# Kernel tuning notes

Measured on AMD Instinct MI355X. Metric: run time of the kernel, lower is better.

The kernel has to match this reference:

```python
import jax, jax.numpy as jnp
import numpy as np

D_MODEL = 1024
NUM_HEADS = 16
HEAD_DIM = D_MODEL // NUM_HEADS


def setup_inputs() -> dict:
    key = jax.random.key(0)
    k1, k2, k3, k4, k5 = jax.random.split(key, 5)
    B, S = 2, 2048
    X = jax.random.normal(k1, (B, S, D_MODEL), dtype=jnp.float32)
    Wqkv = jax.random.normal(k2, (3 * D_MODEL, D_MODEL), dtype=jnp.float32) * 0.02
    bqkv = jax.random.normal(k3, (3 * D_MODEL,), dtype=jnp.float32) * 0.02
    Wo = jax.random.normal(k4, (D_MODEL, D_MODEL), dtype=jnp.float32) * 0.02
    bo = jax.random.normal(k5, (D_MODEL,), dtype=jnp.float32) * 0.02
    return {"X": X, "Wqkv": Wqkv, "bqkv": bqkv, "Wo": Wo, "bo": bo}


def reference(X, Wqkv, bqkv, Wo, bo):
    B, S, D = X.shape
    # fused QKV projection (torch Linear: x @ W.T + b)
    qkv = X @ Wqkv.T + bqkv                                  # [B, S, 3D]
    qkv = qkv.reshape(B, S, NUM_HEADS, 3 * HEAD_DIM)
    qkv = jnp.transpose(qkv, (0, 2, 1, 3))                   # [B, H, S, 3*hd]
    q, k, v = jnp.split(qkv, 3, axis=-1)                     # each [B, H, S, hd]
    # naive scaled dot-product attention (materializes full SxS scores)
    scale = 1.0 / jnp.sqrt(jnp.asarray(HEAD_DIM, dtype=X.dtype))
    scores = jnp.einsum("bhqd,bhkd->bhqk", q, k) * scale     # [B, H, S, S]
    attn = jax.nn.softmax(scores, axis=-1)
    values = jnp.einsum("bhqk,bhkd->bhqd", attn, v)          # [B, H, S, hd]
    values = jnp.transpose(values, (0, 2, 1, 3)).reshape(B, S, D)
    return values @ Wo.T + bo
```

## Files before the change

kernel.cpp:

```cpp
#include <hip/hip_runtime.h>

#define DM    1024
#define NH    16
#define HD    64
#define SEQ   2048
#define BATCH 2
#define NQKV  3072
#define MTOT  4096

using half2v = __attribute__((ext_vector_type(2))) _Float16;
using half4  = __attribute__((ext_vector_type(4))) _Float16;
using half8  = __attribute__((ext_vector_type(8))) _Float16;
using f32x4  = __attribute__((ext_vector_type(4))) float;

typedef const __attribute__((address_space(1))) unsigned int* gp_t;
typedef __attribute__((address_space(3))) unsigned int* lp_t;

__device__ __forceinline__ void gl2lds16(const void* g, void* l) {
    __builtin_amdgcn_global_load_lds((gp_t)g, (lp_t)l, 16, 0, 0);
}

__device__ __forceinline__ f32x4 fzero4() {
    f32x4 v; v[0] = 0.f; v[1] = 0.f; v[2] = 0.f; v[3] = 0.f; return v;
}

__device__ __forceinline__ int sw8(int row, int col) {
    return (row << 6) | ((((col >> 3) ^ row) & 7) << 3) | (col & 7);
}
__device__ __forceinline__ int sw16(int row, int col) {
    return (row << 7) | ((((col >> 3) ^ row) & 15) << 3) | (col & 7);
}

#define CSCALE 0.18033688011112042f

__device__ __forceinline__ half2v expp2(float a, float b) {
    return __builtin_bit_cast(half2v, __builtin_amdgcn_cvt_pkrtz(
        __builtin_amdgcn_exp2f(a), __builtin_amdgcn_exp2f(b)));
}

__global__ __launch_bounds__(256) void cvt_all(const float* __restrict__ X,
                                               const float* __restrict__ W1,
                                               const float* __restrict__ W2,
                                               const float* __restrict__ bqkv,
                                               float* __restrict__ bscaled,
                                               _Float16* __restrict__ out) {
    const int nX = MTOT * DM / 4, nW1 = NQKV * DM / 4, nW2 = DM * DM / 4;
    int i = blockIdx.x * 256 + threadIdx.x;
    if (i < NQKV) {
        const float b = bqkv[i];
        bscaled[i] = ((i % 192) < 64) ? b * CSCALE : b;
    }
    if (i >= nX + nW1 + nW2) return;
    float4 f;
    float sc = 1.0f;
    if (i < nX) {
        f = reinterpret_cast<const float4*>(X)[i];
    } else if (i < nX + nW1) {
        const int off = i - nX;
        f = reinterpret_cast<const float4*>(W1)[off];
        const int row = off >> 8;
        if ((row % 192) < 64) sc = CSCALE;
    } else {
        f = reinterpret_cast<const float4*>(W2)[i - nX - nW1];
    }
    half4 h;
    h[0] = (_Float16)(f.x * sc); h[1] = (_Float16)(f.y * sc);
    h[2] = (_Float16)(f.z * sc); h[3] = (_Float16)(f.w * sc);
    reinterpret_cast<half4*>(out)[i] = h;
}

template <bool OUT_F16>
__global__ __launch_bounds__(256) void gemm_nt(const _Float16* __restrict__ A,
                                               const _Float16* __restrict__ B,
                                               const float* __restrict__ bias,
                                               void* __restrict__ Cout,
                                               int M, int N, int K) {
    __shared__ _Float16 lA[128 * 64];
    __shared__ _Float16 lB[128 * 64];
    const int tid = threadIdx.x;
    const int m0 = blockIdx.y * 128, n0 = blockIdx.x * 128;
    const int wave = tid >> 6, lane = tid & 63, quad = lane >> 4, l15 = lane & 15;
    const int wm = (wave & 1) * 64, wn = (wave >> 1) * 64;

    f32x4 acc[4][4];
#pragma unroll
    for (int i = 0; i < 4; ++i)
#pragma unroll
        for (int j = 0; j < 4; ++j) acc[i][j] = fzero4();

    const int cperm = (((tid & 7) ^ (tid >> 3)) & 7) * 8;
    const _Float16* Ab = A + (long)(m0 + (tid >> 3)) * K + cperm;
    const _Float16* Bb = B + (long)(n0 + (tid >> 3)) * K + cperm;
    char* lAp = (char*)lA + tid * 16;
    char* lBp = (char*)lB + tid * 16;

    for (int kt = 0; kt < K; kt += 64) {
        __syncthreads();
#pragma unroll
        for (int j = 0; j < 4; ++j) {
            gl2lds16(Ab + (long)j * 32 * K + kt, lAp + j * 4096);
            gl2lds16(Bb + (long)j * 32 * K + kt, lBp + j * 4096);
        }
        __syncthreads();
#pragma unroll
        for (int ks = 0; ks < 2; ++ks) {
            half8 af[4], bfr[4];
#pragma unroll
            for (int t = 0; t < 4; ++t) {
                af[t]  = *(const half8*)(lA + sw8(wm + t * 16 + l15, ks * 32 + quad * 8));
                bfr[t] = *(const half8*)(lB + sw8(wn + t * 16 + l15, ks * 32 + quad * 8));
            }
#pragma unroll
            for (int mt = 0; mt < 4; ++mt)
#pragma unroll
                for (int nt = 0; nt < 4; ++nt)
                    acc[mt][nt] = __builtin_amdgcn_mfma_f32_16x16x32_f16(
                        af[mt], bfr[nt], acc[mt][nt], 0, 0, 0);
        }
    }

    float bs[4];
#pragma unroll
    for (int nt = 0; nt < 4; ++nt) bs[nt] = bias[n0 + wn + nt * 16 + l15];

#pragma unroll
    for (int mt = 0; mt < 4; ++mt) {
#pragma unroll
        for (int r = 0; r < 4; ++r) {
            const int m = m0 + wm + mt * 16 + quad * 4 + r;
#pragma unroll
            for (int nt = 0; nt < 4; ++nt) {
                const int n = n0 + wn + nt * 16 + l15;
                const float v = acc[mt][nt][r] + bs[nt];
                if constexpr (OUT_F16)
                    ((_Float16*)Cout)[(long)m * N + n] = (_Float16)v;
                else
                    ((float*)Cout)[(long)m * N + n] = v;
            }
        }
    }
}

template <bool OUT_F16>
__global__ __launch_bounds__(256) void gemm_nt_64(const _Float16* __restrict__ A,
                                                  const _Float16* __restrict__ B,
                                                  const float* __restrict__ bias,
                                                  void* __restrict__ Cout,
                                                  int M, int N, int K) {
    __shared__ _Float16 lA[64 * 64];
    __shared__ _Float16 lB[128 * 64];
    const int tid = threadIdx.x;
    const int m0 = blockIdx.y * 64, n0 = blockIdx.x * 128;
    const int wave = tid >> 6, lane = tid & 63, quad = lane >> 4, l15 = lane & 15;
    const int wm = (wave & 1) * 32, wn = (wave >> 1) * 64;

    f32x4 acc[2][4];
#pragma unroll
    for (int i = 0; i < 2; ++i)
#pragma unroll
        for (int j = 0; j < 4; ++j) acc[i][j] = fzero4();

    const int cperm = (((tid & 7) ^ (tid >> 3)) & 7) * 8;
    const _Float16* Ab = A + (long)(m0 + (tid >> 3)) * K + cperm;
    const _Float16* Bb = B + (long)(n0 + (tid >> 3)) * K + cperm;
    char* lAp = (char*)lA + tid * 16;
    char* lBp = (char*)lB + tid * 16;

    for (int kt = 0; kt < K; kt += 64) {
        __syncthreads();
#pragma unroll
        for (int j = 0; j < 2; ++j)
            gl2lds16(Ab + (long)j * 32 * K + kt, lAp + j * 4096);
#pragma unroll
        for (int j = 0; j < 4; ++j)
            gl2lds16(Bb + (long)j * 32 * K + kt, lBp + j * 4096);
        __syncthreads();
#pragma unroll
        for (int ks = 0; ks < 2; ++ks) {
            half8 af[2], bfr[4];
#pragma unroll
            for (int t = 0; t < 2; ++t)
                af[t] = *(const half8*)(lA + sw8(wm + t * 16 + l15, ks * 32 + quad * 8));
#pragma unroll
            for (int t = 0; t < 4; ++t)
                bfr[t] = *(const half8*)(lB + sw8(wn + t * 16 + l15, ks * 32 + quad * 8));
#pragma unroll
            for (int mt = 0; mt < 2; ++mt)
#pragma unroll
                for (int nt = 0; nt < 4; ++nt)
                    acc[mt][nt] = __builtin_amdgcn_mfma_f32_16x16x32_f16(
                        af[mt], bfr[nt], acc[mt][nt], 0, 0, 0);
        }
    }

    float bs[4];
#pragma unroll
    for (int nt = 0; nt < 4; ++nt) bs[nt] = bias[n0 + wn + nt * 16 + l15];

#pragma unroll
    for (int mt = 0; mt < 2; ++mt) {
#pragma unroll
        for (int r = 0; r < 4; ++r) {
            const int m = m0 + wm + mt * 16 + quad * 4 + r;
#pragma unroll
            for (int nt = 0; nt < 4; ++nt) {
                const int n = n0 + wn + nt * 16 + l15;
                const float v = acc[mt][nt][r] + bs[nt];
                if constexpr (OUT_F16)
                    ((_Float16*)Cout)[(long)m * N + n] = (_Float16)v;
                else
                    ((float*)Cout)[(long)m * N + n] = v;
            }
        }
    }
}

__global__ __launch_bounds__(256) void repack_v(const _Float16* __restrict__ qkvh,
                                                _Float16* __restrict__ vt) {
    const int b = blockIdx.z, h = blockIdx.y, s0 = blockIdx.x * 32;
    const int d = threadIdx.x & 63, si = threadIdx.x >> 6;
    const _Float16* src = qkvh + (long)(b * SEQ + s0 + si * 8) * NQKV + h * 192 + 128 + d;
    half8 v;
#pragma unroll
    for (int i = 0; i < 8; ++i) v[i] = src[(long)i * NQKV];
    *(half8*)(vt + (long)((b * NH + h) * HD + d) * SEQ + s0 + si * 8) = v;
}

__global__ __launch_bounds__(256) void attn_flash(const _Float16* __restrict__ qkv,
                                                  const _Float16* __restrict__ vt,
                                                  _Float16* __restrict__ aout) {
    __shared__ _Float16 lQ[128 * 64];
    __shared__ _Float16 lK[128 * 64];
    __shared__ _Float16 lV[64 * 128];
    const int b = blockIdx.z, h = blockIdx.y, q0 = blockIdx.x * 128;
    const int tid = threadIdx.x;
    const int wave = tid >> 6, lane = tid & 63, quad = lane >> 4, l15 = lane & 15;

    const int cperm8  = (((tid & 7) ^ (tid >> 3)) & 7) * 8;
    const int cperm16 = (((tid & 15) ^ (tid >> 4)) & 15) * 8;

    const _Float16* qsrc = qkv + (long)(b * SEQ + q0 + (tid >> 3)) * NQKV + h * 192 + cperm8;
#pragma unroll
    for (int j = 0; j < 4; ++j)
        gl2lds16(qsrc + (long)j * 32 * NQKV, (char*)lQ + j * 4096 + tid * 16);
    __syncthreads();

    half8 qf[2][2];
#pragma unroll
    for (int qt = 0; qt < 2; ++qt)
#pragma unroll
        for (int ks = 0; ks < 2; ++ks)
            qf[qt][ks] = *(const half8*)(lQ + sw8(wave * 32 + qt * 16 + l15, ks * 32 + quad * 8));

    f32x4 O[2][4];
#pragma unroll
    for (int qt = 0; qt < 2; ++qt)
#pragma unroll
        for (int dt = 0; dt < 4; ++dt) O[qt][dt] = fzero4();
    f32x4 lsum[2] = {fzero4(), fzero4()};

    half8 ones;
#pragma unroll
    for (int i = 0; i < 8; ++i) ones[i] = (_Float16)1.0f;

    const _Float16* ksrc = qkv + (long)(b * SEQ + (tid >> 3)) * NQKV + h * 192 + 64 + cperm8;
    const _Float16* vsrc = vt + (long)((b * NH + h) * HD + (tid >> 4)) * SEQ + cperm16;

    for (int it = 0; it < 16; ++it) {
        const int s0 = it * 128;
        __syncthreads();
#pragma unroll
        for (int j = 0; j < 4; ++j) {
            gl2lds16(ksrc + (long)(s0 + j * 32) * NQKV, (char*)lK + j * 4096 + tid * 16);
            gl2lds16(vsrc + (long)j * 16 * SEQ + s0,    (char*)lV + j * 4096 + tid * 16);
        }
        __syncthreads();

#pragma unroll
        for (int t = 0; t < 4; ++t) {
            f32x4 s[2][2];
            s[0][0] = fzero4(); s[0][1] = fzero4();
            s[1][0] = fzero4(); s[1][1] = fzero4();
#pragma unroll
            for (int tt = 0; tt < 2; ++tt) {
#pragma unroll
                for (int ks = 0; ks < 2; ++ks) {
                    half8 kf = *(const half8*)(lK + sw8((2 * t + tt) * 16 + l15, ks * 32 + quad * 8));
                    s[0][tt] = __builtin_amdgcn_mfma_f32_16x16x32_f16(kf, qf[0][ks], s[0][tt], 0, 0, 0);
                    s[1][tt] = __builtin_amdgcn_mfma_f32_16x16x32_f16(kf, qf[1][ks], s[1][tt], 0, 0, 0);
                }
            }
            half8 pf[2];
#pragma unroll
            for (int qt = 0; qt < 2; ++qt) {
                half2v p01 = expp2(s[qt][0][0], s[qt][0][1]);
                half2v p23 = expp2(s[qt][0][2], s[qt][0][3]);
                half2v p45 = expp2(s[qt][1][0], s[qt][1][1]);
                half2v p67 = expp2(s[qt][1][2], s[qt][1][3]);
                half4 lo = __builtin_shufflevector(p01, p23, 0, 1, 2, 3);
                half4 hi = __builtin_shufflevector(p45, p67, 0, 1, 2, 3);
                pf[qt] = __builtin_shufflevector(lo, hi, 0, 1, 2, 3, 4, 5, 6, 7);
                lsum[qt] = __builtin_amdgcn_mfma_f32_16x16x32_f16(pf[qt], ones, lsum[qt], 0, 0, 0);
            }
#pragma unroll
            for (int dt = 0; dt < 4; ++dt) {
                const int vrow = dt * 16 + l15;
                half4 v0 = *(const half4*)(lV + sw16(vrow, t * 32 + quad * 4));
                half4 v1 = *(const half4*)(lV + sw16(vrow, t * 32 + quad * 4 + 16));
                half8 vf = __builtin_shufflevector(v0, v1, 0, 1, 2, 3, 4, 5, 6, 7);
                O[0][dt] = __builtin_amdgcn_mfma_f32_16x16x32_f16(pf[0], vf, O[0][dt], 0, 0, 0);
                O[1][dt] = __builtin_amdgcn_mfma_f32_16x16x32_f16(pf[1], vf, O[1][dt], 0, 0, 0);
            }
        }
    }

#pragma unroll
    for (int qt = 0; qt < 2; ++qt) {
#pragma unroll
        for (int r = 0; r < 4; ++r) {
            const float lr = 1.0f / lsum[qt][r];
            const int row = b * SEQ + q0 + wave * 32 + qt * 16 + quad * 4 + r;
#pragma unroll
            for (int dt = 0; dt < 4; ++dt)
                aout[(long)row * DM + h * HD + dt * 16 + l15] =
                    (_Float16)(O[qt][dt][r] * lr);
        }
    }
}

extern "C" void kernel_launch(void* const* d_in, const int* in_sizes, int n_in,
                              void* d_out, int out_size, void* d_ws, size_t ws_size,
                              hipStream_t stream) {
    const float* X    = (const float*)d_in[0];
    const float* Wqkv = (const float*)d_in[1];
    const float* bqkv = (const float*)d_in[2];
    const float* Wo   = (const float*)d_in[3];
    const float* bo   = (const float*)d_in[4];

    char* ws = (char*)d_ws;
    _Float16* Xh   = (_Float16*)(ws);
    _Float16* Wqh  = (_Float16*)(ws + (size_t)8  * 1048576);
    _Float16* Woh  = (_Float16*)(ws + (size_t)14 * 1048576);
    _Float16* qkvh = (_Float16*)(ws + (size_t)16 * 1048576);
    _Float16* vth  = (_Float16*)(ws + (size_t)40 * 1048576);
    _Float16* atth = (_Float16*)(ws + (size_t)48 * 1048576);
    float* bscaled = (float*)(ws + (size_t)48 * 1048576);
    (void)Wqh; (void)Woh;

    const int ncvt = (MTOT * DM + NQKV * DM + DM * DM) / 4;
    cvt_all<<<(ncvt + 255) / 256, 256, 0, stream>>>(X, Wqkv, Wo, bqkv, bscaled, Xh);

    gemm_nt<true><<<dim3(NQKV / 128, MTOT / 128), 256, 0, stream>>>(
        Xh, Wqh, bscaled, qkvh, MTOT, NQKV, DM);

    repack_v<<<dim3(SEQ / 32, NH, BATCH), 256, 0, stream>>>(qkvh, vth);

    attn_flash<<<dim3(SEQ / 128, NH, BATCH), 256, 0, stream>>>(qkvh, vth, atth);

    gemm_nt_64<false><<<dim3(DM / 128, MTOT / 64), 256, 0, stream>>>(
        atth, Woh, bo, d_out, MTOT, DM, DM);
}
```

Baseline: 190.5 us.

## Double-buffer K/V tiles in flash attention and remap blocks per XCD

The attention kernel now streams K and V in 64-key tiles into two LDS buffers. It prefetches the next tile while computing the current one, so there is one barrier per iteration instead of two serialized load/compute phases. The V tile now uses the same 8-chunk swizzle as K. Block indices are also remapped so that blocks sharing a (batch, head) pair are grouped onto the same chiplet, which is meant to improve L2 reuse of K/V. The cost is twice as many loop iterations and barriers, with a smaller tile per step.

```diff
diff --git a/kernel.cpp b/kernel.cpp
--- a/kernel.cpp
+++ b/kernel.cpp
@@ -26,9 +26,6 @@
 
 __device__ __forceinline__ int sw8(int row, int col) {
     return (row << 6) | ((((col >> 3) ^ row) & 7) << 3) | (col & 7);
-}
-__device__ __forceinline__ int sw16(int row, int col) {
-    return (row << 7) | ((((col >> 3) ^ row) & 15) << 3) | (col & 7);
 }
 
 #define CSCALE 0.18033688011112042f
@@ -230,19 +227,32 @@
                                                   const _Float16* __restrict__ vt,
                                                   _Float16* __restrict__ aout) {
     __shared__ _Float16 lQ[128 * 64];
-    __shared__ _Float16 lK[128 * 64];
-    __shared__ _Float16 lV[64 * 128];
-    const int b = blockIdx.z, h = blockIdx.y, q0 = blockIdx.x * 128;
+    __shared__ _Float16 lK[2][64 * 64];
+    __shared__ _Float16 lV[2][64 * 64];
+
+    const int L = blockIdx.x + 16 * blockIdx.y + 256 * blockIdx.z;
+    const int c = L & 7, j = L >> 3;
+    const int pair = c * 4 + (j >> 4);
+    const int b = pair >> 4, h = pair & 15;
+    const int q0 = (j & 15) * 128;
+
     const int tid = threadIdx.x;
     const int wave = tid >> 6, lane = tid & 63, quad = lane >> 4, l15 = lane & 15;
-
-    const int cperm8  = (((tid & 7) ^ (tid >> 3)) & 7) * 8;
-    const int cperm16 = (((tid & 15) ^ (tid >> 4)) & 15) * 8;
+    const int cperm8 = (((tid & 7) ^ (tid >> 3)) & 7) * 8;
 
     const _Float16* qsrc = qkv + (long)(b * SEQ + q0 + (tid >> 3)) * NQKV + h * 192 + cperm8;
 #pragma unroll
-    for (int j = 0; j < 4; ++j)
-        gl2lds16(qsrc + (long)j * 32 * NQKV, (char*)lQ + j * 4096 + tid * 16);
+    for (int jq = 0; jq < 4; ++jq)
+        gl2lds16(qsrc + (long)jq * 32 * NQKV, (char*)lQ + jq * 4096 + tid * 16);
+
+    const _Float16* ksrc = qkv + (long)(b * SEQ + (tid >> 3)) * NQKV + h * 192 + 64 + cperm8;
+    const _Float16* vsrc = vt + (long)((b * NH + h) * HD + (tid >> 3)) * SEQ + cperm8;
+
+#pragma unroll
+    for (int jj = 0; jj < 2; ++jj) {
+        gl2lds16(ksrc + (long)(jj * 32) * NQKV, (char*)lK[0] + jj * 4096 + tid * 16);
+        gl2lds16(vsrc + (long)(jj * 32) * SEQ,  (char*)lV[0] + jj * 4096 + tid * 16);
+    }
     __syncthreads();
 
     half8 qf[2][2];
@@ -263,21 +273,19 @@
 #pragma unroll
     for (int i = 0; i < 8; ++i) ones[i] = (_Float16)1.0f;
 
-    const _Float16* ksrc = qkv + (long)(b * SEQ + (tid >> 3)) * NQKV + h * 192 + 64 + cperm8;
-    const _Float16* vsrc = vt + (long)((b * NH + h) * HD + (tid >> 4)) * SEQ + cperm16;
-
-    for (int it = 0; it < 16; ++it) {
-        const int s0 = it * 128;
-        __syncthreads();
-#pragma unroll
-        for (int j = 0; j < 4; ++j) {
-            gl2lds16(ksrc + (long)(s0 + j * 32) * NQKV, (char*)lK + j * 4096 + tid * 16);
-            gl2lds16(vsrc + (long)j * 16 * SEQ + s0,    (char*)lV + j * 4096 + tid * 16);
-        }
-        __syncthreads();
-
-#pragma unroll
-        for (int t = 0; t < 4; ++t) {
+    for (int it = 0; it < 32; ++it) {
+        const int cur = it & 1;
+        if (it < 31) {
+            const int s0n = (it + 1) * 64;
+#pragma unroll
+            for (int jj = 0; jj < 2; ++jj) {
+                gl2lds16(ksrc + (long)(s0n + jj * 32) * NQKV, (char*)lK[cur ^ 1] + jj * 4096 + tid * 16);
+                gl2lds16(vsrc + (long)(jj * 32) * SEQ + s0n,  (char*)lV[cur ^ 1] + jj * 4096 + tid * 16);
+            }
+        }
+
+#pragma unroll
+        for (int t = 0; t < 2; ++t) {
             f32x4 s[2][2];
             s[0][0] = fzero4(); s[0][1] = fzero4();
             s[1][0] = fzero4(); s[1][1] = fzero4();
@@ -285,7 +293,7 @@
             for (int tt = 0; tt < 2; ++tt) {
 #pragma unroll
                 for (int ks = 0; ks < 2; ++ks) {
-                    half8 kf = *(const half8*)(lK + sw8((2 * t + tt) * 16 + l15, ks * 32 + quad * 8));
+                    half8 kf = *(const half8*)(lK[cur] + sw8((2 * t + tt) * 16 + l15, ks * 32 + quad * 8));
                     s[0][tt] = __builtin_amdgcn_mfma_f32_16x16x32_f16(kf, qf[0][ks], s[0][tt], 0, 0, 0);
                     s[1][tt] = __builtin_amdgcn_mfma_f32_16x16x32_f16(kf, qf[1][ks], s[1][tt], 0, 0, 0);
                 }
@@ -305,13 +313,14 @@
 #pragma unroll
             for (int dt = 0; dt < 4; ++dt) {
                 const int vrow = dt * 16 + l15;
-                half4 v0 = *(const half4*)(lV + sw16(vrow, t * 32 + quad * 4));
-                half4 v1 = *(const half4*)(lV + sw16(vrow, t * 32 + quad * 4 + 16));
+                half4 v0 = *(const half4*)(lV[cur] + sw8(vrow, t * 32 + quad * 4));
+                half4 v1 = *(const half4*)(lV[cur] + sw8(vrow, t * 32 + quad * 4 + 16));
                 half8 vf = __builtin_shufflevector(v0, v1, 0, 1, 2, 3, 4, 5, 6, 7);
                 O[0][dt] = __builtin_amdgcn_mfma_f32_16x16x32_f16(pf[0], vf, O[0][dt], 0, 0, 0);
                 O[1][dt] = __builtin_amdgcn_mfma_f32_16x16x32_f16(pf[1], vf, O[1][dt], 0, 0, 0);
             }
         }
+        __syncthreads();
     }
 
 #pragma unroll
@@ -345,7 +354,6 @@
     _Float16* vth  = (_Float16*)(ws + (size_t)40 * 1048576);
     _Float16* atth = (_Float16*)(ws + (size_t)48 * 1048576);
     float* bscaled = (float*)(ws + (size_t)48 * 1048576);
-    (void)Wqh; (void)Woh;
 
     const int ncvt = (MTOT * DM + NQKV * DM + DM * DM) / 4;
     cvt_all<<<(ncvt + 255) / 256, 256, 0, stream>>>(X, Wqkv, Wo, bqkv, bscaled, Xh);
```

After: 196.1 us. +2.9%, slower.
